# Kernel optimization log

Measured on AMD Instinct MI355X. Metric: run time of the kernel, lower is better.

## Reference

```python
import jax, jax.numpy as jnp
import numpy as np

N = 262144  # number of points / sequence length
D = 64      # feature dim (qkv_dim); deterministic features => nb_features == D
KERNEL_EPSILON = 1e-3


def setup_inputs() -> dict:
    key = jax.random.key(0)
    ks = jax.random.split(key, 7)
    s = 1.0 / np.sqrt(D)
    return {
        "x": jax.random.normal(ks[0], (N, D), dtype=jnp.float32),
        "Wq": jax.random.normal(ks[1], (D, D), dtype=jnp.float32) * s,
        "bq": jnp.zeros((D,), dtype=jnp.float32),
        "Wk": jax.random.normal(ks[2], (D, D), dtype=jnp.float32) * s,
        "bk": jnp.zeros((D,), dtype=jnp.float32),
        "Wv": jax.random.normal(ks[3], (D, D), dtype=jnp.float32) * s,
        "bv": jnp.zeros((D,), dtype=jnp.float32),
    }


def reference(x, Wq, bq, Wk, bk, Wv, bv):
    # Dense projections (flax nn.Dense: x @ W + b)
    q = x @ Wq + bq  # [N, D]
    k = x @ Wk + bk
    v = x @ Wv + bv
    # Deterministic generalized kernel feature map: relu(data) + kernel_epsilon
    qp = jax.nn.relu(q) + KERNEL_EPSILON  # [N, M], M == D
    kp = jax.nn.relu(k) + KERNEL_EPSILON  # [N, M]
    # Bidirectional FAVOR+ linear attention: O(N*M*D)
    kv = jnp.einsum("nm,nd->md", kp, v)       # [M, D]
    num = jnp.einsum("nm,md->nd", qp, kv)     # [N, D]
    # renormalize_attention=True: divide by qp . sum(kp)
    denom = qp @ kp.sum(axis=0)               # [N]
    return num / denom[:, None]
```

## Files before the change

### kernel.cpp

```cpp
#include <hip/hip_runtime.h>
#include <hip/hip_bf16.h>


#define NPTS 262144
#define TILES (NPTS / 64)
#define GRID1 512
#define TPB1 (TILES / GRID1)
#define GRID2 512
#define TPB2 (TILES / GRID2)
#define L2STRIDE 4112
#define EPS 1e-3f

typedef __attribute__((ext_vector_type(8))) short short8;
typedef __attribute__((ext_vector_type(4))) float f32x4;

__device__ __forceinline__ unsigned short f2bf(float f) {
    __hip_bfloat16 h = __float2bfloat16(f);
    return __builtin_bit_cast(unsigned short, h);
}

__device__ __forceinline__ short8 cvt8(float4 p0, float4 p1) {
    short8 a;
    a[0] = (short)f2bf(p0.x); a[1] = (short)f2bf(p0.y); a[2] = (short)f2bf(p0.z); a[3] = (short)f2bf(p0.w);
    a[4] = (short)f2bf(p1.x); a[5] = (short)f2bf(p1.y); a[6] = (short)f2bf(p1.z); a[7] = (short)f2bf(p1.w);
    return a;
}

__device__ __forceinline__ void lds_barrier() {
    asm volatile("s_waitcnt lgkmcnt(0)" ::: "memory");
    __builtin_amdgcn_s_barrier();
}

__device__ __forceinline__ void stage_mat(const float* __restrict__ W,
                                          unsigned short (*dst)[72], int srow, int sc0) {
    const float* p = W + srow * 64 + sc0;
    float4 f0 = ((const float4*)p)[0];
    float4 f1 = ((const float4*)p)[1];
    float4 f2 = ((const float4*)p)[2];
    float4 f3 = ((const float4*)p)[3];
    float ff[16] = {f0.x, f0.y, f0.z, f0.w, f1.x, f1.y, f1.z, f1.w,
                    f2.x, f2.y, f2.z, f2.w, f3.x, f3.y, f3.z, f3.w};
    unsigned hh[8];
#pragma unroll
    for (int e = 0; e < 8; ++e)
        hh[e] = (unsigned)f2bf(ff[2 * e]) | ((unsigned)f2bf(ff[2 * e + 1]) << 16);
    uint4 u0 = {hh[0], hh[1], hh[2], hh[3]};
    uint4 u1 = {hh[4], hh[5], hh[6], hh[7]};
    *(uint4*)&dst[srow][sc0] = u0;
    *(uint4*)&dst[srow][sc0 + 8] = u1;
}

__global__ __launch_bounds__(256, 4) void pass1_kernel(
    const float* __restrict__ x,
    const float* __restrict__ Wk, const float* __restrict__ bk,
    const float* __restrict__ Wv, const float* __restrict__ bv,
    float* __restrict__ kvPart, float* __restrict__ ksPart)
{
    __shared__ unsigned short kpT[64][72];
    __shared__ unsigned short vT[64][72];
    __shared__ unsigned short wkF[8][64][8];
    __shared__ unsigned short wvF[8][64][8];

    const int tid = threadIdx.x;
    const int w = tid >> 6, l = tid & 63, l15 = l & 15, lg = l >> 4;
    const int srow = tid >> 2, sc0 = (tid & 3) * 16;

    {
        const float* Ws[2] = {Wk, Wv};
        unsigned short (*Fs[2])[64][8] = {wkF, wvF};
#pragma unroll
        for (int m = 0; m < 2; ++m) {
            stage_mat(Ws[m], kpT, srow, sc0);
            __syncthreads();
#pragma unroll
            for (int kk = 0; kk < 2; ++kk) {
                short8 t;
#pragma unroll
                for (int e = 0; e < 8; ++e)
                    t[e] = (short)kpT[kk * 32 + lg * 8 + e][w * 16 + l15];
                *(short8*)&Fs[m][w * 2 + kk][l][0] = t;
            }
            __syncthreads();
        }
    }
    float bkl[4], bvl[4];
#pragma unroll
    for (int j = 0; j < 4; ++j) { bkl[j] = bk[j * 16 + l15]; bvl[j] = bv[j * 16 + l15]; }

    f32x4 akv[4];
#pragma unroll
    for (int j = 0; j < 4; ++j) akv[j] = (f32x4){0.f, 0.f, 0.f, 0.f};
    float ks[4] = {0.f, 0.f, 0.f, 0.f};

    const int t0 = blockIdx.x * TPB1;
    const float* xbase = x + ((size_t)t0 * 64 + w * 16 + l15) * 64 + lg * 8;
    float4 c0 = *(const float4*)(xbase + 0);
    float4 c1 = *(const float4*)(xbase + 4);
    float4 c2 = *(const float4*)(xbase + 32);
    float4 c3 = *(const float4*)(xbase + 36);
    const int nbase = w * 16 + lg * 4;

    for (int t = 0; t < TPB1; ++t) {
        const float* xn = xbase + (size_t)((t + 1 < TPB1) ? (t + 1) : t) * 4096;
        float4 n0 = *(const float4*)(xn + 0);
        float4 n1 = *(const float4*)(xn + 4);
        float4 n2 = *(const float4*)(xn + 32);
        float4 n3 = *(const float4*)(xn + 36);

        short8 a0 = cvt8(c0, c1);
        short8 a1 = cvt8(c2, c3);

#pragma unroll
        for (int j = 0; j < 4; ++j) {
            short8 bk0 = *(const short8*)&wkF[j * 2 + 0][l][0];
            short8 bk1 = *(const short8*)&wkF[j * 2 + 1][l][0];
            short8 bv0 = *(const short8*)&wvF[j * 2 + 0][l][0];
            short8 bv1 = *(const short8*)&wvF[j * 2 + 1][l][0];
            f32x4 z = (f32x4){0.f, 0.f, 0.f, 0.f};
            f32x4 ak = __builtin_amdgcn_mfma_f32_16x16x32_bf16(a0, bk0, z, 0, 0, 0);
            ak = __builtin_amdgcn_mfma_f32_16x16x32_bf16(a1, bk1, ak, 0, 0, 0);
            f32x4 av = __builtin_amdgcn_mfma_f32_16x16x32_bf16(a0, bv0, z, 0, 0, 0);
            av = __builtin_amdgcn_mfma_f32_16x16x32_bf16(a1, bv1, av, 0, 0, 0);
            unsigned short h[4], g[4];
#pragma unroll
            for (int r = 0; r < 4; ++r) {
                float kp = fmaxf(ak[r] + bkl[j], 0.f) + EPS;
                ks[j] += kp;
                h[r] = f2bf(kp);
                g[r] = f2bf(av[r] + bvl[j]);
            }
            uint2 hp = {(unsigned)h[0] | ((unsigned)h[1] << 16), (unsigned)h[2] | ((unsigned)h[3] << 16)};
            uint2 gp = {(unsigned)g[0] | ((unsigned)g[1] << 16), (unsigned)g[2] | ((unsigned)g[3] << 16)};
            *(uint2*)&kpT[j * 16 + l15][nbase] = hp;
            *(uint2*)&vT[j * 16 + l15][nbase] = gp;
        }
        lds_barrier();
        short8 ka0 = *(const short8*)&kpT[w * 16 + l15][lg * 8];
        short8 ka1 = *(const short8*)&kpT[w * 16 + l15][32 + lg * 8];
#pragma unroll
        for (int j = 0; j < 4; ++j) {
            short8 vb0 = *(const short8*)&vT[j * 16 + l15][lg * 8];
            short8 vb1 = *(const short8*)&vT[j * 16 + l15][32 + lg * 8];
            akv[j] = __builtin_amdgcn_mfma_f32_16x16x32_bf16(ka0, vb0, akv[j], 0, 0, 0);
            akv[j] = __builtin_amdgcn_mfma_f32_16x16x32_bf16(ka1, vb1, akv[j], 0, 0, 0);
        }
        lds_barrier();
        c0 = n0; c1 = n1; c2 = n2; c3 = n3;
    }

    float* kvs = kvPart + (size_t)blockIdx.x * 4096;
#pragma unroll
    for (int j = 0; j < 4; ++j)
#pragma unroll
        for (int r = 0; r < 4; ++r)
            kvs[(size_t)(w * 16 + lg * 4 + r) * 64 + j * 16 + l15] = akv[j][r];
#pragma unroll
    for (int j = 0; j < 4; ++j) {
        float s = ks[j];
        s += __shfl_xor(s, 16, 64);
        s += __shfl_xor(s, 32, 64);
        if (lg == 0) ksPart[(size_t)blockIdx.x * 256 + w * 64 + j * 16 + l15] = s;
    }
}

__global__ __launch_bounds__(256, 4) void reduceA_kernel(
    const float* __restrict__ kvPart, const float* __restrict__ ksPart,
    float* __restrict__ l2kv, float* __restrict__ l2ks)
{
    const int b = blockIdx.x, t = threadIdx.x;
    if (b < 64) {
        f32x4 acc[4];
#pragma unroll
        for (int si = 0; si < 4; ++si) acc[si] = (f32x4){0.f, 0.f, 0.f, 0.f};
        const float* base = kvPart + (size_t)b * 8 * 4096;
#pragma unroll
        for (int r = 0; r < 8; ++r)
#pragma unroll
            for (int si = 0; si < 4; ++si)
                acc[si] += *(const f32x4*)(base + (size_t)r * 4096 + si * 1024 + t * 4);
#pragma unroll
        for (int si = 0; si < 4; ++si)
            *(f32x4*)(l2kv + (size_t)b * L2STRIDE + si * 1024 + t * 4) = acc[si];
    } else {
        const int i = b - 64;
        float acc = 0.f;
        const float* p = ksPart + (size_t)i * 128 * 256 + t;
#pragma unroll 8
        for (int r = 0; r < 128; ++r) acc += p[(size_t)r * 256];
        l2ks[i * 256 + t] = acc;
    }
}

__global__ __launch_bounds__(256, 4) void reduceB_kernel(
    const float* __restrict__ l2kv, const float* __restrict__ l2ks,
    float* __restrict__ kvFin, float* __restrict__ ksFin)
{
    const int b = blockIdx.x, t = threadIdx.x;
    if (b < 4) {
        f32x4 acc = (f32x4){0.f, 0.f, 0.f, 0.f};
        const float* p = l2kv + b * 1024 + t * 4;
#pragma unroll 8
        for (int s = 0; s < 64; ++s) acc += *(const f32x4*)(p + (size_t)s * L2STRIDE);
        *(f32x4*)(kvFin + b * 1024 + t * 4) = acc;
    } else if (t < 64) {
        float s = 0.f;
#pragma unroll
        for (int i = 0; i < 16; ++i) s += l2ks[i * 64 + t];
        ksFin[t] = s;
    }
}

__global__ __launch_bounds__(256, 2) void pass2_kernel(
    const float* __restrict__ x, const float* __restrict__ Wq, const float* __restrict__ bq,
    const float* __restrict__ kvFin, const float* __restrict__ ksFin,
    float* __restrict__ out)
{
    __shared__ unsigned short stageS[64][72];
    __shared__ unsigned short wqF[8][64][8];

    const int tid = threadIdx.x;
    const int w = tid >> 6, l = tid & 63, l15 = l & 15, lg = l >> 4;
    const int srow = tid >> 2, sc0 = (tid & 3) * 16;

    stage_mat(Wq, stageS, srow, sc0);
    __syncthreads();
    {
#pragma unroll
        for (int kk = 0; kk < 2; ++kk) {
            short8 t;
#pragma unroll
            for (int e = 0; e < 8; ++e)
                t[e] = (short)stageS[kk * 32 + lg * 8 + e][w * 16 + l15];
            *(short8*)&wqF[w * 2 + kk][l][0] = t;
        }
    }
    __syncthreads();
    stage_mat(kvFin, stageS, srow, sc0);
    __syncthreads();
    short8 kvA[4][2];
#pragma unroll
    for (int dj = 0; dj < 4; ++dj)
#pragma unroll
        for (int kk = 0; kk < 2; ++kk) {
            short8 t;
#pragma unroll
            for (int e = 0; e < 8; ++e) {
                int m = (kk * 2 + (e >> 2)) * 16 + lg * 4 + (e & 3);
                t[e] = (short)stageS[m][dj * 16 + l15];
            }
            kvA[dj][kk] = t;
        }
    float bql2[4][4], ksl2[4][4];
#pragma unroll
    for (int jm = 0; jm < 4; ++jm)
#pragma unroll
        for (int r = 0; r < 4; ++r) {
            bql2[jm][r] = bq[jm * 16 + lg * 4 + r];
            ksl2[jm][r] = ksFin[jm * 16 + lg * 4 + r];
        }

    const int t0 = blockIdx.x * TPB2;
    const float* xbase = x + ((size_t)t0 * 64 + w * 16 + l15) * 64 + lg * 8;
    float4 c0 = *(const float4*)(xbase + 0);
    float4 c1 = *(const float4*)(xbase + 4);
    float4 c2 = *(const float4*)(xbase + 32);
    float4 c3 = *(const float4*)(xbase + 36);

    for (int t = 0; t < TPB2; ++t) {
        const float* xn = xbase + (size_t)((t + 1 < TPB2) ? (t + 1) : t) * 4096;
        float4 n0 = *(const float4*)(xn + 0);
        float4 n1 = *(const float4*)(xn + 4);
        float4 n2 = *(const float4*)(xn + 32);
        float4 n3 = *(const float4*)(xn + 36);

        short8 a0 = cvt8(c0, c1);
        short8 a1 = cvt8(c2, c3);

        const f32x4 z = (f32x4){0.f, 0.f, 0.f, 0.f};
        float dp = 0.f;
        short8 qb0, qb1;
#pragma unroll
        for (int jm = 0; jm < 4; ++jm) {
            short8 wq0 = *(const short8*)&wqF[jm * 2 + 0][l][0];
            short8 wq1 = *(const short8*)&wqF[jm * 2 + 1][l][0];
            f32x4 aq = __builtin_amdgcn_mfma_f32_16x16x32_bf16(wq0, a0, z, 0, 0, 0);
            aq = __builtin_amdgcn_mfma_f32_16x16x32_bf16(wq1, a1, aq, 0, 0, 0);
#pragma unroll
            for (int r = 0; r < 4; ++r) {
                float qv = fmaxf(aq[r] + bql2[jm][r], 0.f) + EPS;
                dp += qv * ksl2[jm][r];
                unsigned short h = f2bf(qv);
                if (jm < 2) qb0[(jm & 1) * 4 + r] = (short)h;
                else        qb1[(jm & 1) * 4 + r] = (short)h;
            }
        }
        dp += __shfl_xor(dp, 16, 64);
        dp += __shfl_xor(dp, 32, 64);
        const float inv = __builtin_amdgcn_rcpf(dp);

        const size_t nrow = (size_t)(t0 + t) * 64 + w * 16 + l15;
#pragma unroll
        for (int dj = 0; dj < 4; ++dj) {
            f32x4 nm = __builtin_amdgcn_mfma_f32_16x16x32_bf16(kvA[dj][0], qb0, z, 0, 0, 0);
            nm = __builtin_amdgcn_mfma_f32_16x16x32_bf16(kvA[dj][1], qb1, nm, 0, 0, 0);
            f32x4 o4 = {nm[0] * inv, nm[1] * inv, nm[2] * inv, nm[3] * inv};
            *(f32x4*)(out + nrow * 64 + dj * 16 + lg * 4) = o4;
        }
        c0 = n0; c1 = n1; c2 = n2; c3 = n3;
    }
}

extern "C" void kernel_launch(void* const* d_in, const int* in_sizes, int n_in,
                              void* d_out, int out_size, void* d_ws, size_t ws_size,
                              hipStream_t stream)
{
    const float* x  = (const float*)d_in[0];
    const float* Wq = (const float*)d_in[1];
    const float* bq = (const float*)d_in[2];
    const float* Wk = (const float*)d_in[3];
    const float* bk = (const float*)d_in[4];
    const float* Wv = (const float*)d_in[5];
    const float* bv = (const float*)d_in[6];
    float* out = (float*)d_out;

    float* kvPart = (float*)d_ws;
    float* ksPart = kvPart + (size_t)GRID1 * 4096;
    float* l2kv   = ksPart + (size_t)GRID1 * 256;
    float* l2ks   = l2kv + (size_t)64 * L2STRIDE;
    float* kvFin  = l2ks + 4 * 256;
    float* ksFin  = kvFin + 4096;

    hipLaunchKernelGGL(pass1_kernel, dim3(GRID1), dim3(256), 0, stream,
                       x, Wk, bk, Wv, bv, kvPart, ksPart);
    hipLaunchKernelGGL(reduceA_kernel, dim3(68), dim3(256), 0, stream,
                       kvPart, ksPart, l2kv, l2ks);
    hipLaunchKernelGGL(reduceB_kernel, dim3(5), dim3(256), 0, stream,
                       l2kv, l2ks, kvFin, ksFin);
    hipLaunchKernelGGL(pass2_kernel, dim3(GRID2), dim3(256), 0, stream,
                       x, Wq, bq, kvFin, ksFin, out);
}
```

Baseline: 58.53 us.

## Process two x tiles per iteration in pass1 with double LDS buffers

Pass1 now handles two 64-row tiles per loop iteration. Each has its own LDS kp/v buffer, so two tiles share one pair of barriers and the prefetch covers two tiles ahead. This halves barrier count per tile and raises instruction-level parallelism across independent MFMA chains. The cost is more registers and LDS, reflected in dropping launch bounds occupancy from 4 to 2 blocks per CU. The float-to-bf16 conversion is also replaced with a manual round-to-nearest-even bit trick, which skips NaN handling.

Result: no change. 57.75 us (-1.3%).

```diff
diff --git a/kernel.cpp b/kernel.cpp
--- a/kernel.cpp
+++ b/kernel.cpp
@@ -6,6 +6,7 @@
 #define TILES (NPTS / 64)
 #define GRID1 512
 #define TPB1 (TILES / GRID1)
+#define PAIRS (TPB1 / 2)
 #define GRID2 512
 #define TPB2 (TILES / GRID2)
 #define L2STRIDE 4112
@@ -15,8 +16,9 @@
 typedef __attribute__((ext_vector_type(4))) float f32x4;
 
 __device__ __forceinline__ unsigned short f2bf(float f) {
-    __hip_bfloat16 h = __float2bfloat16(f);
-    return __builtin_bit_cast(unsigned short, h);
+    unsigned u = __builtin_bit_cast(unsigned, f);
+    u += 0x7FFFu + ((u >> 16) & 1u);
+    return (unsigned short)(u >> 16);
 }
 
 __device__ __forceinline__ short8 cvt8(float4 p0, float4 p1) {
@@ -50,14 +52,14 @@
     *(uint4*)&dst[srow][sc0 + 8] = u1;
 }
 
-__global__ __launch_bounds__(256, 4) void pass1_kernel(
+__global__ __launch_bounds__(256, 2) void pass1_kernel(
     const float* __restrict__ x,
     const float* __restrict__ Wk, const float* __restrict__ bk,
     const float* __restrict__ Wv, const float* __restrict__ bv,
     float* __restrict__ kvPart, float* __restrict__ ksPart)
 {
-    __shared__ unsigned short kpT[64][72];
-    __shared__ unsigned short vT[64][72];
+    __shared__ unsigned short kpT[2][64][72];
+    __shared__ unsigned short vT[2][64][72];
     __shared__ unsigned short wkF[8][64][8];
     __shared__ unsigned short wvF[8][64][8];
 
@@ -70,14 +72,14 @@
         unsigned short (*Fs[2])[64][8] = {wkF, wvF};
 #pragma unroll
         for (int m = 0; m < 2; ++m) {
-            stage_mat(Ws[m], kpT, srow, sc0);
+            stage_mat(Ws[m], kpT[0], srow, sc0);
             __syncthreads();
 #pragma unroll
             for (int kk = 0; kk < 2; ++kk) {
                 short8 t;
 #pragma unroll
                 for (int e = 0; e < 8; ++e)
-                    t[e] = (short)kpT[kk * 32 + lg * 8 + e][w * 16 + l15];
+                    t[e] = (short)kpT[0][kk * 32 + lg * 8 + e][w * 16 + l15];
                 *(short8*)&Fs[m][w * 2 + kk][l][0] = t;
             }
             __syncthreads();
@@ -94,21 +96,28 @@
 
     const int t0 = blockIdx.x * TPB1;
     const float* xbase = x + ((size_t)t0 * 64 + w * 16 + l15) * 64 + lg * 8;
-    float4 c0 = *(const float4*)(xbase + 0);
-    float4 c1 = *(const float4*)(xbase + 4);
-    float4 c2 = *(const float4*)(xbase + 32);
-    float4 c3 = *(const float4*)(xbase + 36);
+    float4 cA0 = *(const float4*)(xbase + 0);
+    float4 cA1 = *(const float4*)(xbase + 4);
+    float4 cA2 = *(const float4*)(xbase + 32);
+    float4 cA3 = *(const float4*)(xbase + 36);
+    float4 cB0 = *(const float4*)(xbase + 4096 + 0);
+    float4 cB1 = *(const float4*)(xbase + 4096 + 4);
+    float4 cB2 = *(const float4*)(xbase + 4096 + 32);
+    float4 cB3 = *(const float4*)(xbase + 4096 + 36);
     const int nbase = w * 16 + lg * 4;
 
-    for (int t = 0; t < TPB1; ++t) {
-        const float* xn = xbase + (size_t)((t + 1 < TPB1) ? (t + 1) : t) * 4096;
-        float4 n0 = *(const float4*)(xn + 0);
-        float4 n1 = *(const float4*)(xn + 4);
-        float4 n2 = *(const float4*)(xn + 32);
-        float4 n3 = *(const float4*)(xn + 36);
-
-        short8 a0 = cvt8(c0, c1);
-        short8 a1 = cvt8(c2, c3);
+    for (int p = 0; p < PAIRS; ++p) {
+        short8 a0A = cvt8(cA0, cA1), a1A = cvt8(cA2, cA3);
+        short8 a0B = cvt8(cB0, cB1), a1B = cvt8(cB2, cB3);
+        const float* xn = xbase + (size_t)((p + 1 < PAIRS) ? (p + 1) : p) * 8192;
+        cA0 = *(const float4*)(xn + 0);
+        cA1 = *(const float4*)(xn + 4);
+        cA2 = *(const float4*)(xn + 32);
+        cA3 = *(const float4*)(xn + 36);
+        cB0 = *(const float4*)(xn + 4096 + 0);
+        cB1 = *(const float4*)(xn + 4096 + 4);
+        cB2 = *(const float4*)(xn + 4096 + 32);
+        cB3 = *(const float4*)(xn + 4096 + 36);
 
 #pragma unroll
         for (int j = 0; j < 4; ++j) {
@@ -117,35 +126,47 @@
             short8 bv0 = *(const short8*)&wvF[j * 2 + 0][l][0];
             short8 bv1 = *(const short8*)&wvF[j * 2 + 1][l][0];
             f32x4 z = (f32x4){0.f, 0.f, 0.f, 0.f};
-            f32x4 ak = __builtin_amdgcn_mfma_f32_16x16x32_bf16(a0, bk0, z, 0, 0, 0);
-            ak = __builtin_amdgcn_mfma_f32_16x16x32_bf16(a1, bk1, ak, 0, 0, 0);
-            f32x4 av = __builtin_amdgcn_mfma_f32_16x16x32_bf16(a0, bv0, z, 0, 0, 0);
-            av = __builtin_amdgcn_mfma_f32_16x16x32_bf16(a1, bv1, av, 0, 0, 0);
-            unsigned short h[4], g[4];
+            f32x4 akA = __builtin_amdgcn_mfma_f32_16x16x32_bf16(a0A, bk0, z, 0, 0, 0);
+            akA = __builtin_amdgcn_mfma_f32_16x16x32_bf16(a1A, bk1, akA, 0, 0, 0);
+            f32x4 avA = __builtin_amdgcn_mfma_f32_16x16x32_bf16(a0A, bv0, z, 0, 0, 0);
+            avA = __builtin_amdgcn_mfma_f32_16x16x32_bf16(a1A, bv1, avA, 0, 0, 0);
+            f32x4 akB = __builtin_amdgcn_mfma_f32_16x16x32_bf16(a0B, bk0, z, 0, 0, 0);
+            akB = __builtin_amdgcn_mfma_f32_16x16x32_bf16(a1B, bk1, akB, 0, 0, 0);
+            f32x4 avB = __builtin_amdgcn_mfma_f32_16x16x32_bf16(a0B, bv0, z, 0, 0, 0);
+            avB = __builtin_amdgcn_mfma_f32_16x16x32_bf16(a1B, bv1, avB, 0, 0, 0);
+            unsigned short hA[4], gA[4], hB[4], gB[4];
 #pragma unroll
             for (int r = 0; r < 4; ++r) {
-                float kp = fmaxf(ak[r] + bkl[j], 0.f) + EPS;
-                ks[j] += kp;
-                h[r] = f2bf(kp);
-                g[r] = f2bf(av[r] + bvl[j]);
-            }
-            uint2 hp = {(unsigned)h[0] | ((unsigned)h[1] << 16), (unsigned)h[2] | ((unsigned)h[3] << 16)};
-            uint2 gp = {(unsigned)g[0] | ((unsigned)g[1] << 16), (unsigned)g[2] | ((unsigned)g[3] << 16)};
-            *(uint2*)&kpT[j * 16 + l15][nbase] = hp;
-            *(uint2*)&vT[j * 16 + l15][nbase] = gp;
+                float kA = fmaxf(akA[r] + bkl[j], 0.f) + EPS;
+                float kB = fmaxf(akB[r] + bkl[j], 0.f) + EPS;
+                ks[j] += kA + kB;
+                hA[r] = f2bf(kA); hB[r] = f2bf(kB);
+                gA[r] = f2bf(avA[r] + bvl[j]);
+                gB[r] = f2bf(avB[r] + bvl[j]);
+            }
+            uint2 hpA = {(unsigned)hA[0] | ((unsigned)hA[1] << 16), (unsigned)hA[2] | ((unsigned)hA[3] << 16)};
+            uint2 gpA = {(unsigned)gA[0] | ((unsigned)gA[1] << 16), (unsigned)gA[2] | ((unsigned)gA[3] << 16)};
+            uint2 hpB = {(unsigned)hB[0] | ((unsigned)hB[1] << 16), (unsigned)hB[2] | ((unsigned)hB[3] << 16)};
+            uint2 gpB = {(unsigned)gB[0] | ((unsigned)gB[1] << 16), (unsigned)gB[2] | ((unsigned)gB[3] << 16)};
+            *(uint2*)&kpT[0][j * 16 + l15][nbase] = hpA;
+            *(uint2*)&vT[0][j * 16 + l15][nbase] = gpA;
+            *(uint2*)&kpT[1][j * 16 + l15][nbase] = hpB;
+            *(uint2*)&vT[1][j * 16 + l15][nbase] = gpB;
         }
         lds_barrier();
-        short8 ka0 = *(const short8*)&kpT[w * 16 + l15][lg * 8];
-        short8 ka1 = *(const short8*)&kpT[w * 16 + l15][32 + lg * 8];
-#pragma unroll
-        for (int j = 0; j < 4; ++j) {
-            short8 vb0 = *(const short8*)&vT[j * 16 + l15][lg * 8];
-            short8 vb1 = *(const short8*)&vT[j * 16 + l15][32 + lg * 8];
-            akv[j] = __builtin_amdgcn_mfma_f32_16x16x32_bf16(ka0, vb0, akv[j], 0, 0, 0);
-            akv[j] = __builtin_amdgcn_mfma_f32_16x16x32_bf16(ka1, vb1, akv[j], 0, 0, 0);
+#pragma unroll
+        for (int buf = 0; buf < 2; ++buf) {
+            short8 ka0 = *(const short8*)&kpT[buf][w * 16 + l15][lg * 8];
+            short8 ka1 = *(const short8*)&kpT[buf][w * 16 + l15][32 + lg * 8];
+#pragma unroll
+            for (int j = 0; j < 4; ++j) {
+                short8 vb0 = *(const short8*)&vT[buf][j * 16 + l15][lg * 8];
+                short8 vb1 = *(const short8*)&vT[buf][j * 16 + l15][32 + lg * 8];
+                akv[j] = __builtin_amdgcn_mfma_f32_16x16x32_bf16(ka0, vb0, akv[j], 0, 0, 0);
+                akv[j] = __builtin_amdgcn_mfma_f32_16x16x32_bf16(ka1, vb1, akv[j], 0, 0, 0);
+            }
         }
         lds_barrier();
-        c0 = n0; c1 = n1; c2 = n2; c3 = n3;
     }
 
     float* kvs = kvPart + (size_t)blockIdx.x * 4096;
```

## Keep kp/v in registers and accumulate full kv per wave, reduce across waves

Applied to the files above, without the earlier changes.

Pass 1 previously wrote kp and v tiles to LDS transposed and then read them back, with two barriers per tile, to form the kp^T·v MFMA operands. Now each wave feeds its own MFMA output registers, repacked, directly as operands and keeps a full 64x64 kv accumulator (16 f32x4 per lane). The four waves' partials are combined through LDS in a tree at the end. This removes the per-tile LDS traffic and barriers, but it raises register pressure, so launch bounds drop from 4 to 3 blocks per CU, and f2bf becomes a hand-written round-to-nearest-even bit trick.

Result: slower. 72.78 us (+24.3%).

```diff
diff --git a/kernel.cpp b/kernel.cpp
--- a/kernel.cpp
+++ b/kernel.cpp
@@ -15,8 +15,9 @@
 typedef __attribute__((ext_vector_type(4))) float f32x4;
 
 __device__ __forceinline__ unsigned short f2bf(float f) {
-    __hip_bfloat16 h = __float2bfloat16(f);
-    return __builtin_bit_cast(unsigned short, h);
+    unsigned u = __builtin_bit_cast(unsigned, f);
+    u += 0x7FFFu + ((u >> 16) & 1u);
+    return (unsigned short)(u >> 16);
 }
 
 __device__ __forceinline__ short8 cvt8(float4 p0, float4 p1) {
@@ -24,11 +25,6 @@
     a[0] = (short)f2bf(p0.x); a[1] = (short)f2bf(p0.y); a[2] = (short)f2bf(p0.z); a[3] = (short)f2bf(p0.w);
     a[4] = (short)f2bf(p1.x); a[5] = (short)f2bf(p1.y); a[6] = (short)f2bf(p1.z); a[7] = (short)f2bf(p1.w);
     return a;
-}
-
-__device__ __forceinline__ void lds_barrier() {
-    asm volatile("s_waitcnt lgkmcnt(0)" ::: "memory");
-    __builtin_amdgcn_s_barrier();
 }
 
 __device__ __forceinline__ void stage_mat(const float* __restrict__ W,
@@ -50,16 +46,15 @@
     *(uint4*)&dst[srow][sc0 + 8] = u1;
 }
 
-__global__ __launch_bounds__(256, 4) void pass1_kernel(
+__global__ __launch_bounds__(256, 3) void pass1_kernel(
     const float* __restrict__ x,
     const float* __restrict__ Wk, const float* __restrict__ bk,
     const float* __restrict__ Wv, const float* __restrict__ bv,
     float* __restrict__ kvPart, float* __restrict__ ksPart)
 {
-    __shared__ unsigned short kpT[64][72];
-    __shared__ unsigned short vT[64][72];
-    __shared__ unsigned short wkF[8][64][8];
-    __shared__ unsigned short wvF[8][64][8];
+    __shared__ unsigned short stageS[64][72];
+    __shared__ unsigned short wF[16][64][8];
+    float* red = (float*)&wF[0][0][0];
 
     const int tid = threadIdx.x;
     const int w = tid >> 6, l = tid & 63, l15 = l & 15, lg = l >> 4;
@@ -67,18 +62,17 @@
 
     {
         const float* Ws[2] = {Wk, Wv};
-        unsigned short (*Fs[2])[64][8] = {wkF, wvF};
 #pragma unroll
         for (int m = 0; m < 2; ++m) {
-            stage_mat(Ws[m], kpT, srow, sc0);
+            stage_mat(Ws[m], stageS, srow, sc0);
             __syncthreads();
 #pragma unroll
             for (int kk = 0; kk < 2; ++kk) {
                 short8 t;
 #pragma unroll
                 for (int e = 0; e < 8; ++e)
-                    t[e] = (short)kpT[kk * 32 + lg * 8 + e][w * 16 + l15];
-                *(short8*)&Fs[m][w * 2 + kk][l][0] = t;
+                    t[e] = (short)stageS[kk * 32 + lg * 8 + e][w * 16 + l15];
+                *(short8*)&wF[m * 8 + w * 2 + kk][l][0] = t;
             }
             __syncthreads();
         }
@@ -87,9 +81,11 @@
 #pragma unroll
     for (int j = 0; j < 4; ++j) { bkl[j] = bk[j * 16 + l15]; bvl[j] = bv[j * 16 + l15]; }
 
-    f32x4 akv[4];
-#pragma unroll
-    for (int j = 0; j < 4; ++j) akv[j] = (f32x4){0.f, 0.f, 0.f, 0.f};
+    f32x4 akv[4][4];
+#pragma unroll
+    for (int jm = 0; jm < 4; ++jm)
+#pragma unroll
+        for (int jd = 0; jd < 4; ++jd) akv[jm][jd] = (f32x4){0.f, 0.f, 0.f, 0.f};
     float ks[4] = {0.f, 0.f, 0.f, 0.f};
 
     const int t0 = blockIdx.x * TPB1;
@@ -98,7 +94,6 @@
     float4 c1 = *(const float4*)(xbase + 4);
     float4 c2 = *(const float4*)(xbase + 32);
     float4 c3 = *(const float4*)(xbase + 36);
-    const int nbase = w * 16 + lg * 4;
 
     for (int t = 0; t < TPB1; ++t) {
         const float* xn = xbase + (size_t)((t + 1 < TPB1) ? (t + 1) : t) * 4096;
@@ -110,50 +105,96 @@
         short8 a0 = cvt8(c0, c1);
         short8 a1 = cvt8(c2, c3);
 
+        short8 kpf[4], vf[4];
 #pragma unroll
         for (int j = 0; j < 4; ++j) {
-            short8 bk0 = *(const short8*)&wkF[j * 2 + 0][l][0];
-            short8 bk1 = *(const short8*)&wkF[j * 2 + 1][l][0];
-            short8 bv0 = *(const short8*)&wvF[j * 2 + 0][l][0];
-            short8 bv1 = *(const short8*)&wvF[j * 2 + 1][l][0];
+            short8 bk0 = *(const short8*)&wF[0 + j * 2 + 0][l][0];
+            short8 bk1 = *(const short8*)&wF[0 + j * 2 + 1][l][0];
+            short8 bv0 = *(const short8*)&wF[8 + j * 2 + 0][l][0];
+            short8 bv1 = *(const short8*)&wF[8 + j * 2 + 1][l][0];
             f32x4 z = (f32x4){0.f, 0.f, 0.f, 0.f};
             f32x4 ak = __builtin_amdgcn_mfma_f32_16x16x32_bf16(a0, bk0, z, 0, 0, 0);
             ak = __builtin_amdgcn_mfma_f32_16x16x32_bf16(a1, bk1, ak, 0, 0, 0);
             f32x4 av = __builtin_amdgcn_mfma_f32_16x16x32_bf16(a0, bv0, z, 0, 0, 0);
             av = __builtin_amdgcn_mfma_f32_16x16x32_bf16(a1, bv1, av, 0, 0, 0);
-            unsigned short h[4], g[4];
+            short8 kc = (short8){0, 0, 0, 0, 0, 0, 0, 0};
+            short8 vc = (short8){0, 0, 0, 0, 0, 0, 0, 0};
 #pragma unroll
             for (int r = 0; r < 4; ++r) {
                 float kp = fmaxf(ak[r] + bkl[j], 0.f) + EPS;
                 ks[j] += kp;
-                h[r] = f2bf(kp);
-                g[r] = f2bf(av[r] + bvl[j]);
+                kc[r] = (short)f2bf(kp);
+                vc[r] = (short)f2bf(av[r] + bvl[j]);
             }
-            uint2 hp = {(unsigned)h[0] | ((unsigned)h[1] << 16), (unsigned)h[2] | ((unsigned)h[3] << 16)};
-            uint2 gp = {(unsigned)g[0] | ((unsigned)g[1] << 16), (unsigned)g[2] | ((unsigned)g[3] << 16)};
-            *(uint2*)&kpT[j * 16 + l15][nbase] = hp;
-            *(uint2*)&vT[j * 16 + l15][nbase] = gp;
-        }
-        lds_barrier();
-        short8 ka0 = *(const short8*)&kpT[w * 16 + l15][lg * 8];
-        short8 ka1 = *(const short8*)&kpT[w * 16 + l15][32 + lg * 8];
-#pragma unroll
-        for (int j = 0; j < 4; ++j) {
-            short8 vb0 = *(const short8*)&vT[j * 16 + l15][lg * 8];
-            short8 vb1 = *(const short8*)&vT[j * 16 + l15][32 + lg * 8];
-            akv[j] = __builtin_amdgcn_mfma_f32_16x16x32_bf16(ka0, vb0, akv[j], 0, 0, 0);
-            akv[j] = __builtin_amdgcn_mfma_f32_16x16x32_bf16(ka1, vb1, akv[j], 0, 0, 0);
-        }
-        lds_barrier();
+            kpf[j] = kc; vf[j] = vc;
+        }
+#pragma unroll
+        for (int jm = 0; jm < 4; ++jm)
+#pragma unroll
+            for (int jd = 0; jd < 4; ++jd)
+                akv[jm][jd] = __builtin_amdgcn_mfma_f32_16x16x32_bf16(kpf[jm], vf[jd], akv[jm][jd], 0, 0, 0);
+
         c0 = n0; c1 = n1; c2 = n2; c3 = n3;
     }
 
-    float* kvs = kvPart + (size_t)blockIdx.x * 4096;
-#pragma unroll
-    for (int j = 0; j < 4; ++j)
-#pragma unroll
-        for (int r = 0; r < 4; ++r)
-            kvs[(size_t)(w * 16 + lg * 4 + r) * 64 + j * 16 + l15] = akv[j][r];
+#define KV_IDX(jm, jd, r) ((size_t)((jm) * 16 + lg * 4 + (r)) * 64 + (jd) * 16 + l15)
+    __syncthreads();
+    if (w == 1) {
+#pragma unroll
+        for (int jm = 0; jm < 4; ++jm)
+#pragma unroll
+            for (int jd = 0; jd < 4; ++jd)
+#pragma unroll
+                for (int r = 0; r < 4; ++r) red[KV_IDX(jm, jd, r)] = akv[jm][jd][r];
+    }
+    __syncthreads();
+    if (w == 0) {
+#pragma unroll
+        for (int jm = 0; jm < 4; ++jm)
+#pragma unroll
+            for (int jd = 0; jd < 4; ++jd)
+#pragma unroll
+                for (int r = 0; r < 4; ++r) akv[jm][jd][r] += red[KV_IDX(jm, jd, r)];
+    }
+    __syncthreads();
+    if (w == 3) {
+#pragma unroll
+        for (int jm = 0; jm < 4; ++jm)
+#pragma unroll
+            for (int jd = 0; jd < 4; ++jd)
+#pragma unroll
+                for (int r = 0; r < 4; ++r) red[KV_IDX(jm, jd, r)] = akv[jm][jd][r];
+    }
+    __syncthreads();
+    if (w == 2) {
+#pragma unroll
+        for (int jm = 0; jm < 4; ++jm)
+#pragma unroll
+            for (int jd = 0; jd < 4; ++jd)
+#pragma unroll
+                for (int r = 0; r < 4; ++r) akv[jm][jd][r] += red[KV_IDX(jm, jd, r)];
+    }
+    __syncthreads();
+    if (w == 2) {
+#pragma unroll
+        for (int jm = 0; jm < 4; ++jm)
+#pragma unroll
+            for (int jd = 0; jd < 4; ++jd)
+#pragma unroll
+                for (int r = 0; r < 4; ++r) red[KV_IDX(jm, jd, r)] = akv[jm][jd][r];
+    }
+    __syncthreads();
+    if (w == 0) {
+        float* kvs = kvPart + (size_t)blockIdx.x * 4096;
+#pragma unroll
+        for (int jm = 0; jm < 4; ++jm)
+#pragma unroll
+            for (int jd = 0; jd < 4; ++jd)
+#pragma unroll
+                for (int r = 0; r < 4; ++r)
+                    kvs[KV_IDX(jm, jd, r)] = akv[jm][jd][r] + red[KV_IDX(jm, jd, r)];
+    }
+#undef KV_IDX
 #pragma unroll
     for (int j = 0; j < 4; ++j) {
         float s = ks[j];
```
